# Kernel optimization log

Measured on AMD Instinct MI355X. Metric: run time of the kernel, lower is better.

## Reference

```python
import jax, jax.numpy as jnp
import numpy as np

N_DET, N_T, NY, NX, B = 128, 2048, 256, 256, 4


def setup_inputs() -> dict:
    key = jax.random.key(0)
    k1, k2, k3 = jax.random.split(key, 3)
    sino = jax.random.normal(k1, (B, 1, N_DET, N_T), dtype=jnp.float32)
    # lut[..., 0]: fractional time-of-flight index in [0, n_t-1)
    tof = jax.random.uniform(k2, (NY, NX, N_DET), dtype=jnp.float32) * (N_T - 1)
    # lut[..., 1]: linear-interp fraction alpha in [0, 1)
    alpha = jax.random.uniform(k3, (NY, NX, N_DET), dtype=jnp.float32)
    lut = jnp.stack([tof, alpha], axis=-1)  # [ny, nx, n_det, 2]
    return {"sino": sino, "lut": lut}


def reference(sino, lut):
    b, _, n_det, n_t = sino.shape
    ny, nx = lut.shape[0], lut.shape[1]
    P = ny * nx

    # Precompute (as in __init__): floor index, validity mask, interp fraction.
    k_floor = jnp.floor(lut[..., 0])
    valid = (k_floor >= 0) & (k_floor < n_t - 1)
    k0 = jnp.clip(k_floor, 0, max(n_t - 2, 0)).astype(jnp.int32)  # [ny,nx,n_det]
    alpha = lut[..., 1]

    # Hann apodization window over detectors (non-trainable buffer).
    apod = (0.5 - 0.5 * jnp.cos(
        2.0 * jnp.pi * jnp.arange(n_det, dtype=jnp.float32) / max(n_det - 1, 1)
    )).astype(sino.dtype)

    S = sino[:, 0]  # [B, n_det, n_t]

    # Move detector axis first so we can gather all detectors at once.
    k0t = k0.reshape(P, n_det).T          # [n_det, P]
    at = alpha.reshape(P, n_det).T        # [n_det, P]
    vt = valid.reshape(P, n_det).T.astype(sino.dtype)  # [n_det, P]

    s0 = jnp.take_along_axis(S, k0t[None], axis=2)        # [B, n_det, P]
    s1 = jnp.take_along_axis(S, (k0t + 1)[None], axis=2)  # [B, n_det, P]
    sk = ((1.0 - at) * s0 + at * s1) * vt                  # masked lerp

    out = jnp.einsum('d,bdp->bp', apod, sk)                # apodized reduce over detectors
    norm = jnp.maximum(apod.sum(), jnp.finfo(apod.dtype).tiny)
    return (out / norm).reshape(b, 1, ny, nx)
```

## Files before the change

### kernel.cpp

```cpp
#include <hip/hip_runtime.h>
#include <hip/hip_fp16.h>

#define N_DET 128
#define N_T   2048
#define NPIX  65536
#define NBATCH 4
#define G 8
#define PT 1024
#define NGB (N_DET / G)

typedef float f4_t __attribute__((ext_vector_type(4)));

__global__ __launch_bounds__(256) void sino_pack_kernel(
    const float* __restrict__ sino, float2* __restrict__ ws) {
  const int idx = blockIdx.x * blockDim.x + threadIdx.x;
  const __half2 lo = __floats2half2_rn(
      __builtin_nontemporal_load(sino + 0 * N_DET * N_T + idx),
      __builtin_nontemporal_load(sino + 1 * N_DET * N_T + idx));
  const __half2 hi = __floats2half2_rn(
      __builtin_nontemporal_load(sino + 2 * N_DET * N_T + idx),
      __builtin_nontemporal_load(sino + 3 * N_DET * N_T + idx));
  union { struct { __half2 a, b; } h; float2 f; } u;
  u.h.a = lo;
  u.h.b = hi;
  ws[idx] = u.f;
}

__global__ __launch_bounds__(1024, 4) void das_lds_kernel(
    const float* __restrict__ lut, const float2* __restrict__ ws,
    float* __restrict__ out) {
  __shared__ float2 sino_s[G * N_T];

  const int tid = threadIdx.x;
  const int tile = blockIdx.x;
  const int g = blockIdx.y;
  const int p = tile * PT + tid;

  const f4_t* lp =
      reinterpret_cast<const f4_t*>(lut + ((size_t)p * N_DET + g * G) * 2);
  f4_t l[4];
#pragma unroll
  for (int j = 0; j < 4; ++j) l[j] = __builtin_nontemporal_load(lp + j);

  {
    const float4* src = reinterpret_cast<const float4*>(ws + (size_t)g * G * N_T);
    float4* dst = reinterpret_cast<float4*>(sino_s);
#pragma unroll
    for (int i = 0; i < 8192 / 1024; ++i) dst[tid + i * 1024] = src[tid + i * 1024];
  }

  float apd[G];
#pragma unroll
  for (int j = 0; j < G; ++j) {
    apd[j] = 0.5f - 0.5f * cosf(6.28318530717958647692f *
                                ((float)(g * G + j) / (float)(N_DET - 1)));
  }
  __syncthreads();

  float a0 = 0.f, a1 = 0.f, a2 = 0.f, a3 = 0.f;
#pragma unroll
  for (int j = 0; j < G; ++j) {
    const float tof = (j & 1) ? l[j >> 1].z : l[j >> 1].x;
    const float al  = (j & 1) ? l[j >> 1].w : l[j >> 1].y;
    const float kf = floorf(tof);
    const bool valid = (kf >= 0.0f) && (kf < (float)(N_T - 1));
    const float kcl = fminf(fmaxf(kf, 0.0f), (float)(N_T - 2));
    const int k0 = (int)kcl;
    const float w = valid ? apd[j] : 0.0f;

    const float2 r0 = sino_s[j * N_T + k0];
    const float2 r1 = sino_s[j * N_T + k0 + 1];
    const __half2* h0 = reinterpret_cast<const __half2*>(&r0);
    const __half2* h1 = reinterpret_cast<const __half2*>(&r1);
    const float2 s0a = __half22float2(h0[0]);
    const float2 s0b = __half22float2(h0[1]);
    const float2 s1a = __half22float2(h1[0]);
    const float2 s1b = __half22float2(h1[1]);

    a0 += w * (s0a.x + al * (s1a.x - s0a.x));
    a1 += w * (s0a.y + al * (s1a.y - s0a.y));
    a2 += w * (s0b.x + al * (s1b.x - s0b.x));
    a3 += w * (s0b.y + al * (s1b.y - s0b.y));
  }

  const float nrm = 1.0f / 63.5f;
  atomicAdd(out + 0 * NPIX + p, a0 * nrm);
  atomicAdd(out + 1 * NPIX + p, a1 * nrm);
  atomicAdd(out + 2 * NPIX + p, a2 * nrm);
  atomicAdd(out + 3 * NPIX + p, a3 * nrm);
}

__global__ __launch_bounds__(256) void das_fallback_kernel(
    const float* __restrict__ lut, const float* __restrict__ S,
    float* __restrict__ out) {
  const int lane = threadIdx.x & 63;
  const int p = blockIdx.x * 4 + (threadIdx.x >> 6);

  const float4 lv =
      reinterpret_cast<const float4*>(lut + (size_t)p * 2 * N_DET)[lane];

  float acc0 = 0.f, acc1 = 0.f, acc2 = 0.f, acc3 = 0.f;
  float wsum = 0.f;

#pragma unroll
  for (int j = 0; j < 2; ++j) {
    const int d = 2 * lane + j;
    const float tof = j ? lv.z : lv.x;
    const float a   = j ? lv.w : lv.y;
    const float kf = floorf(tof);
    const bool valid = (kf >= 0.0f) && (kf < (float)(N_T - 1));
    const float kcl = fminf(fmaxf(kf, 0.0f), (float)(N_T - 2));
    const int k0 = (int)kcl;
    const float apd =
        0.5f - 0.5f * cosf(6.28318530717958647692f *
                           (1.0f / (float)(N_DET - 1)) * (float)d);
    wsum += apd;
    const float w = valid ? apd : 0.0f;
    const float om = 1.0f - a;
    const float* row = S + (size_t)d * N_T + k0;
    acc0 += w * (om * row[0 * N_DET * N_T] + a * row[0 * N_DET * N_T + 1]);
    acc1 += w * (om * row[1 * N_DET * N_T] + a * row[1 * N_DET * N_T + 1]);
    acc2 += w * (om * row[2 * N_DET * N_T] + a * row[2 * N_DET * N_T + 1]);
    acc3 += w * (om * row[3 * N_DET * N_T] + a * row[3 * N_DET * N_T + 1]);
  }

#pragma unroll
  for (int off = 32; off > 0; off >>= 1) {
    acc0 += __shfl_xor(acc0, off);
    acc1 += __shfl_xor(acc1, off);
    acc2 += __shfl_xor(acc2, off);
    acc3 += __shfl_xor(acc3, off);
    wsum += __shfl_xor(wsum, off);
  }

  if (lane == 0) {
    const float inv = 1.0f / fmaxf(wsum, 1.17549435e-38f);
    out[0 * NPIX + p] = acc0 * inv;
    out[1 * NPIX + p] = acc1 * inv;
    out[2 * NPIX + p] = acc2 * inv;
    out[3 * NPIX + p] = acc3 * inv;
  }
}

extern "C" void kernel_launch(void* const* d_in, const int* in_sizes, int n_in,
                              void* d_out, int out_size, void* d_ws, size_t ws_size,
                              hipStream_t stream) {
  const float* sino = (const float*)d_in[0];
  const float* lut  = (const float*)d_in[1];
  float* out = (float*)d_out;

  const size_t need = (size_t)N_DET * N_T * 8;
  if (ws_size >= need) {
    hipMemsetAsync(d_out, 0, (size_t)out_size * sizeof(float), stream);
    float2* ws = (float2*)d_ws;
    sino_pack_kernel<<<(N_DET * N_T) / 256, 256, 0, stream>>>(sino, ws);
    dim3 grid(NPIX / PT, NGB);
    das_lds_kernel<<<grid, 1024, 0, stream>>>(lut, ws, out);
  } else {
    das_fallback_kernel<<<NPIX / 4, 256, 0, stream>>>(lut, sino, out);
  }
}
```

Baseline: 145.2 us.

## Loop over detector groups per block with double-buffered LDS, drop atomics and memset

Replaces the 2D grid with one block per 256-pixel tile that loops over all 32 detector groups of 4. The next group's packed sinogram is prefetched into registers and stored into a second LDS buffer while the current group is processed. Four threads share each pixel and combine results with lane shuffles, then write once with nontemporal stores. This removes the output memset and the global atomics. In exchange, every block re-reads the whole 2 MB packed sinogram, syncs once per iteration, and gives each thread only one detector per iteration, so less work per thread to hide latency.

```diff
diff --git a/kernel.cpp b/kernel.cpp
--- a/kernel.cpp
+++ b/kernel.cpp
@@ -4,10 +4,10 @@
 #define N_DET 128
 #define N_T   2048
 #define NPIX  65536
-#define NBATCH 4
-#define G 8
-#define PT 1024
-#define NGB (N_DET / G)
+#define G 4
+#define NITER (N_DET / G)
+#define PT 256
+#define TPB 1024
 
 typedef float f4_t __attribute__((ext_vector_type(4)));
 
@@ -26,50 +26,60 @@
   ws[idx] = u.f;
 }
 
-__global__ __launch_bounds__(1024, 4) void das_lds_kernel(
+__global__ __launch_bounds__(TPB, 4) void das_kloop_kernel(
     const float* __restrict__ lut, const float2* __restrict__ ws,
     float* __restrict__ out) {
-  __shared__ float2 sino_s[G * N_T];
+  __shared__ float2 sbuf[2][G * N_T];
+  __shared__ float apod_s[N_DET];
 
   const int tid = threadIdx.x;
-  const int tile = blockIdx.x;
-  const int g = blockIdx.y;
-  const int p = tile * PT + tid;
+  const int px_l = tid >> 2;
+  const int slot = tid & 3;
+  const int p = blockIdx.x * PT + px_l;
 
-  const f4_t* lp =
-      reinterpret_cast<const f4_t*>(lut + ((size_t)p * N_DET + g * G) * 2);
-  f4_t l[4];
-#pragma unroll
-  for (int j = 0; j < 4; ++j) l[j] = __builtin_nontemporal_load(lp + j);
+  if (tid < N_DET) {
+    apod_s[tid] = 0.5f - 0.5f * cosf(6.28318530717958647692f *
+                                     ((float)tid / (float)(N_DET - 1)));
+  }
 
   {
-    const float4* src = reinterpret_cast<const float4*>(ws + (size_t)g * G * N_T);
-    float4* dst = reinterpret_cast<float4*>(sino_s);
+    const float4* src = reinterpret_cast<const float4*>(ws);
+    float4* dst = reinterpret_cast<float4*>(&sbuf[0][0]);
 #pragma unroll
-    for (int i = 0; i < 8192 / 1024; ++i) dst[tid + i * 1024] = src[tid + i * 1024];
+    for (int i = 0; i < 4; ++i) dst[tid + i * TPB] = src[tid + i * TPB];
   }
 
-  float apd[G];
-#pragma unroll
-  for (int j = 0; j < G; ++j) {
-    apd[j] = 0.5f - 0.5f * cosf(6.28318530717958647692f *
-                                ((float)(g * G + j) / (float)(N_DET - 1)));
-  }
+  const float2* lutp =
+      reinterpret_cast<const float2*>(lut) + (size_t)p * N_DET + slot;
+  float2 lcur = lutp[0];
+
   __syncthreads();
 
   float a0 = 0.f, a1 = 0.f, a2 = 0.f, a3 = 0.f;
+
+  for (int g = 0; g < NITER; ++g) {
+    const bool more = (g + 1 < NITER);
+
+    float4 st[4];
+    float2 lnext;
+    if (more) {
+      const float4* src =
+          reinterpret_cast<const float4*>(ws + (size_t)(g + 1) * G * N_T);
 #pragma unroll
-  for (int j = 0; j < G; ++j) {
-    const float tof = (j & 1) ? l[j >> 1].z : l[j >> 1].x;
-    const float al  = (j & 1) ? l[j >> 1].w : l[j >> 1].y;
+      for (int i = 0; i < 4; ++i) st[i] = src[tid + i * TPB];
+      lnext = lutp[(size_t)(g + 1) * G];
+    }
+
+    const float2* sb = sbuf[g & 1];
+    const float tof = lcur.x;
+    const float al = lcur.y;
     const float kf = floorf(tof);
     const bool valid = (kf >= 0.0f) && (kf < (float)(N_T - 1));
-    const float kcl = fminf(fmaxf(kf, 0.0f), (float)(N_T - 2));
-    const int k0 = (int)kcl;
-    const float w = valid ? apd[j] : 0.0f;
+    const int k0 = (int)fminf(fmaxf(kf, 0.0f), (float)(N_T - 2));
+    const float w = valid ? apod_s[g * G + slot] : 0.0f;
 
-    const float2 r0 = sino_s[j * N_T + k0];
-    const float2 r1 = sino_s[j * N_T + k0 + 1];
+    const float2 r0 = sb[slot * N_T + k0];
+    const float2 r1 = sb[slot * N_T + k0 + 1];
     const __half2* h0 = reinterpret_cast<const __half2*>(&r0);
     const __half2* h1 = reinterpret_cast<const __half2*>(&r1);
     const float2 s0a = __half22float2(h0[0]);
@@ -81,13 +91,28 @@
     a1 += w * (s0a.y + al * (s1a.y - s0a.y));
     a2 += w * (s0b.x + al * (s1b.x - s0b.x));
     a3 += w * (s0b.y + al * (s1b.y - s0b.y));
+
+    if (more) {
+      float4* dst = reinterpret_cast<float4*>(&sbuf[(g + 1) & 1][0]);
+#pragma unroll
+      for (int i = 0; i < 4; ++i) dst[tid + i * TPB] = st[i];
+      lcur = lnext;
+    }
+    __syncthreads();
   }
 
-  const float nrm = 1.0f / 63.5f;
-  atomicAdd(out + 0 * NPIX + p, a0 * nrm);
-  atomicAdd(out + 1 * NPIX + p, a1 * nrm);
-  atomicAdd(out + 2 * NPIX + p, a2 * nrm);
-  atomicAdd(out + 3 * NPIX + p, a3 * nrm);
+  a0 += __shfl_xor(a0, 1);  a0 += __shfl_xor(a0, 2);
+  a1 += __shfl_xor(a1, 1);  a1 += __shfl_xor(a1, 2);
+  a2 += __shfl_xor(a2, 1);  a2 += __shfl_xor(a2, 2);
+  a3 += __shfl_xor(a3, 1);  a3 += __shfl_xor(a3, 2);
+
+  if (slot == 0) {
+    const float nrm = 1.0f / 63.5f;
+    __builtin_nontemporal_store(a0 * nrm, out + 0 * NPIX + p);
+    __builtin_nontemporal_store(a1 * nrm, out + 1 * NPIX + p);
+    __builtin_nontemporal_store(a2 * nrm, out + 2 * NPIX + p);
+    __builtin_nontemporal_store(a3 * nrm, out + 3 * NPIX + p);
+  }
 }
 
 __global__ __launch_bounds__(256) void das_fallback_kernel(
@@ -151,11 +176,9 @@
 
   const size_t need = (size_t)N_DET * N_T * 8;
   if (ws_size >= need) {
-    hipMemsetAsync(d_out, 0, (size_t)out_size * sizeof(float), stream);
     float2* ws = (float2*)d_ws;
     sino_pack_kernel<<<(N_DET * N_T) / 256, 256, 0, stream>>>(sino, ws);
-    dim3 grid(NPIX / PT, NGB);
-    das_lds_kernel<<<grid, 1024, 0, stream>>>(lut, ws, out);
+    das_kloop_kernel<<<NPIX / PT, TPB, 0, stream>>>(lut, ws, out);
   } else {
     das_fallback_kernel<<<NPIX / 4, 256, 0, stream>>>(lut, sino, out);
   }
```

Result: faster. 124.9 us (-14.0%).
